# Performance work log

Measured on AMD Instinct MI355X. Metric: run time of the kernel, lower is better.

Reference implementation:

```python
import jax, jax.numpy as jnp
import numpy as np
import math

B, S, N_EMBD, HEAD_SIZE = 32, 2048, 64, 64

def setup_inputs() -> dict:
    key = jax.random.key(0)
    k1, k2, k3, k4 = jax.random.split(key, 4)
    inputs = jax.random.normal(k1, (B, S, N_EMBD), dtype=jnp.float32)
    # nn.Linear(n_embd, head_size, bias=False) weights: shape (head_size, n_embd)
    scale = 1.0 / math.sqrt(N_EMBD)
    Wq = jax.random.normal(k2, (HEAD_SIZE, N_EMBD), dtype=jnp.float32) * scale
    Wk = jax.random.normal(k3, (HEAD_SIZE, N_EMBD), dtype=jnp.float32) * scale
    Wv = jax.random.normal(k4, (HEAD_SIZE, N_EMBD), dtype=jnp.float32) * scale
    return {"inputs": inputs, "Wq": Wq, "Wk": Wk, "Wv": Wv}

def reference(inputs, Wq, Wk, Wv):
    # q, k, v: [B, S, head_size]
    q = jnp.einsum('bse,he->bsh', inputs, Wq)
    k = jnp.einsum('bse,he->bsh', inputs, Wk)
    v = jnp.einsum('bse,he->bsh', inputs, Wv)
    scores = jnp.einsum('bqh,bkh->bqk', q, k) / jnp.sqrt(jnp.float32(HEAD_SIZE))
    # NOTE: the original torch code calls scores.masked_fill(...) out-of-place
    # and discards the result, so NO causal mask is actually applied.
    attention = jax.nn.softmax(scores, axis=-1)
    out = jnp.einsum('bqk,bkh->bqh', attention, v)  # [B, S, head_size]
    return out
```

## Files before the change

kernel.cpp:

```cpp
#include <hip/hip_runtime.h>


#define BATCH 32
#define SEQ   2048
#define HS    64
#define QSCALE 0.18033688011112042f
#define OTS   72
#define MSTR  68

typedef _Float16 f16x8 __attribute__((ext_vector_type(8)));
typedef _Float16 f16x4 __attribute__((ext_vector_type(4)));
typedef float    f32x4 __attribute__((ext_vector_type(4)));
typedef unsigned int u32x4 __attribute__((ext_vector_type(4)));

__global__ __launch_bounds__(256) void prep_w(
    const float* __restrict__ Wq, const float* __restrict__ Wk,
    const float* __restrict__ Wv, _Float16* __restrict__ Wh)
{
    int i = blockIdx.x * 256 + threadIdx.x;
    int rep = i / 12288;
    int j = i - rep * 12288;
    const float* src = (j < 4096) ? Wq : ((j < 8192) ? Wk : Wv);
    float scale = (j < 4096) ? QSCALE : 1.0f;
    Wh[i] = (_Float16)(src[j & 4095] * scale);
}

__global__ __launch_bounds__(256) void proj_kernel(
    const float* __restrict__ x, const _Float16* __restrict__ Wh,
    _Float16* __restrict__ Qh, _Float16* __restrict__ Kh,
    _Float16* __restrict__ Vt)
{
    __shared__ __align__(16) _Float16 ot[64 * OTS];

    const int t    = threadIdx.x;
    const int w    = t >> 6;
    const int lane = t & 63;
    const int lo   = lane & 15;
    const int quad = lane >> 4;
    const long blk0 = (long)blockIdx.x * 64;
    const int  b    = (int)(blk0 / SEQ);
    const int  s0   = (int)(blk0 % SEQ);
    const long rw   = blk0 + w * 16;
    const _Float16* Wrep = Wh + (blockIdx.x & 7) * 12288;

    const float* xp = x + (rw + lo) * HS + quad * 8;
    float4 x0 = *(const float4*)xp;
    float4 x1 = *(const float4*)(xp + 4);
    float4 x2 = *(const float4*)(xp + 32);
    float4 x3 = *(const float4*)(xp + 36);
    f16x8 xb0, xb1;
    xb0[0]=(_Float16)x0.x; xb0[1]=(_Float16)x0.y; xb0[2]=(_Float16)x0.z; xb0[3]=(_Float16)x0.w;
    xb0[4]=(_Float16)x1.x; xb0[5]=(_Float16)x1.y; xb0[6]=(_Float16)x1.z; xb0[7]=(_Float16)x1.w;
    xb1[0]=(_Float16)x2.x; xb1[1]=(_Float16)x2.y; xb1[2]=(_Float16)x2.z; xb1[3]=(_Float16)x2.w;
    xb1[4]=(_Float16)x3.x; xb1[5]=(_Float16)x3.y; xb1[6]=(_Float16)x3.z; xb1[7]=(_Float16)x3.w;

#pragma unroll
    for (int m = 0; m < 3; ++m) {
        const _Float16* Wm = Wrep + m * 4096;
        f32x4 acc[4];
#pragma unroll
        for (int nt = 0; nt < 4; ++nt) { acc[nt][0]=0.f; acc[nt][1]=0.f; acc[nt][2]=0.f; acc[nt][3]=0.f; }
#pragma unroll
        for (int nt = 0; nt < 4; ++nt) {
            f16x8 wa0 = *(const f16x8*)(Wm + (nt * 16 + lo) * 64 + quad * 8);
            f16x8 wa1 = *(const f16x8*)(Wm + (nt * 16 + lo) * 64 + 32 + quad * 8);
            acc[nt] = __builtin_amdgcn_mfma_f32_16x16x32_f16(wa0, xb0, acc[nt], 0, 0, 0);
            acc[nt] = __builtin_amdgcn_mfma_f32_16x16x32_f16(wa1, xb1, acc[nt], 0, 0, 0);
        }
        if (m < 2) {
            _Float16* dst = (m == 0) ? Qh : Kh;
#pragma unroll
            for (int nt = 0; nt < 4; ++nt) {
                f16x4 pk;
                pk[0]=(_Float16)acc[nt][0]; pk[1]=(_Float16)acc[nt][1];
                pk[2]=(_Float16)acc[nt][2]; pk[3]=(_Float16)acc[nt][3];
                *(f16x4*)(dst + (rw + lo) * HS + nt * 16 + quad * 4) = pk;
            }
        } else {
#pragma unroll
            for (int nt = 0; nt < 4; ++nt)
#pragma unroll
                for (int r = 0; r < 4; ++r)
                    ot[(nt * 16 + quad * 4 + r) * OTS + w * 16 + lo] = (_Float16)acc[nt][r];
            __syncthreads();
            const int row = t >> 2, c = t & 3;
            f16x8 r0 = *(const f16x8*)(ot + row * OTS + c * 16);
            f16x8 r1 = *(const f16x8*)(ot + row * OTS + c * 16 + 8);
            _Float16* vd = Vt + ((long)b * HS + row) * SEQ + s0 + c * 16;
            *(f16x8*)vd       = r0;
            *(f16x8*)(vd + 8) = r1;
        }
    }
}

__global__ __launch_bounds__(256, 2) void attn_kernel(
    const _Float16* __restrict__ Q, const _Float16* __restrict__ K,
    const _Float16* __restrict__ Vt, float* __restrict__ out)
{
    __shared__ __align__(16) char smem[65536];
    _Float16* KVb  = (_Float16*)smem;
    float*    obuf = (float*)smem;
    float*    lbuf = obuf + 128 * MSTR;

    const int t    = threadIdx.x;
    const int w    = t >> 6;
    const int lane = t & 63;
    const int lo   = lane & 15;
    const int quad = lane >> 4;
    const int sr   = t >> 2, sc = t & 3;
    const int xr   = lo & 7;

    const int bid = blockIdx.x;
    const int b   = (bid & 7) | ((bid >> 7) << 3);
    const int qt  = (bid >> 3) & 15;
    const int q0  = qt * 128;
    const int qh  = w >> 1;
    const int kh  = w & 1;

    const _Float16* Qb = Q + ((long)b * SEQ + q0 + qh * 64) * HS;
    f16x8 qf[4][2];
#pragma unroll
    for (int q2 = 0; q2 < 4; ++q2) {
        qf[q2][0] = *(const f16x8*)(Qb + (q2 * 16 + lo) * HS + quad * 8);
        qf[q2][1] = *(const f16x8*)(Qb + (q2 * 16 + lo) * HS + 32 + quad * 8);
    }

    const _Float16* Kb = K  + (long)b * SEQ * HS;
    const _Float16* Vb = Vt + (long)b * HS * SEQ;

    const int pr  = (sr & 32) | ((sr & 4) << 2) | ((sr & 24) >> 1) | (sr & 3);
    const int kw0 = pr * 64 + (((2 * sc    ) ^ (pr & 7)) << 3);
    const int kw1 = pr * 64 + (((2 * sc + 1) ^ (pr & 7)) << 3);
    const int vw0 = 4096 + sr * 64 + (((2 * sc    ) ^ (sr & 7)) << 3);
    const int vw1 = 4096 + sr * 64 + (((2 * sc + 1) ^ (sr & 7)) << 3);

    const int kr0 = (kh * 32      + lo) * 64;
    const int kr1 = (kh * 32 + 16 + lo) * 64;
    const int g0  = ((quad    ) ^ xr) << 3;
    const int g1  = ((4 + quad) ^ xr) << 3;
    int voff[4];
#pragma unroll
    for (int ht = 0; ht < 4; ++ht)
        voff[ht] = 4096 + (ht * 16 + lo) * 64 + (((kh * 4 + quad) ^ xr) << 3);

    f32x4 o[4][4], ol[4];
#pragma unroll
    for (int q2 = 0; q2 < 4; ++q2) {
        ol[q2][0]=0.f; ol[q2][1]=0.f; ol[q2][2]=0.f; ol[q2][3]=0.f;
#pragma unroll
        for (int ht = 0; ht < 4; ++ht) { o[q2][ht][0]=0.f; o[q2][ht][1]=0.f; o[q2][ht][2]=0.f; o[q2][ht][3]=0.f; }
    }
    f32x4 zz; zz[0]=0.f; zz[1]=0.f; zz[2]=0.f; zz[3]=0.f;
    f16x8 ones;
#pragma unroll
    for (int j = 0; j < 8; ++j) ones[j] = (_Float16)1.0f;

    const int phase = qt << 1;
    const int key0 = (phase & 31) << 6;
    f16x8 kfA0 = *(const f16x8*)(Kb + (long)(key0 + sr) * HS + sc * 16);
    f16x8 kfB0 = *(const f16x8*)(Kb + (long)(key0 + sr) * HS + sc * 16 + 8);
    f16x8 vfA0 = *(const f16x8*)(Vb + (long)sr * SEQ + key0 + sc * 16);
    f16x8 vfB0 = *(const f16x8*)(Vb + (long)sr * SEQ + key0 + sc * 16 + 8);
    f16x8 kfA1 = *(const f16x8*)(Kb + (long)(key0 + 64 + sr) * HS + sc * 16);
    f16x8 kfB1 = *(const f16x8*)(Kb + (long)(key0 + 64 + sr) * HS + sc * 16 + 8);
    f16x8 vfA1 = *(const f16x8*)(Vb + (long)sr * SEQ + key0 + 64 + sc * 16);
    f16x8 vfB1 = *(const f16x8*)(Vb + (long)sr * SEQ + key0 + 64 + sc * 16 + 8);

    for (int kt2 = 0; kt2 < 16; ++kt2) {
        _Float16* Bp = KVb + (kt2 & 1) * 16384;
        *(f16x8*)(Bp + kw0) = kfA0;
        *(f16x8*)(Bp + kw1) = kfB0;
        *(f16x8*)(Bp + vw0) = vfA0;
        *(f16x8*)(Bp + vw1) = vfB0;
        *(f16x8*)(Bp + 8192 + kw0) = kfA1;
        *(f16x8*)(Bp + 8192 + kw1) = kfB1;
        *(f16x8*)(Bp + 8192 + vw0) = vfA1;
        *(f16x8*)(Bp + 8192 + vw1) = vfB1;

        const int keyn = ((2 * kt2 + 2 + phase) & 31) << 6;
        kfA0 = *(const f16x8*)(Kb + (long)(keyn + sr) * HS + sc * 16);
        kfB0 = *(const f16x8*)(Kb + (long)(keyn + sr) * HS + sc * 16 + 8);
        vfA0 = *(const f16x8*)(Vb + (long)sr * SEQ + keyn + sc * 16);
        vfB0 = *(const f16x8*)(Vb + (long)sr * SEQ + keyn + sc * 16 + 8);
        kfA1 = *(const f16x8*)(Kb + (long)(keyn + 64 + sr) * HS + sc * 16);
        kfB1 = *(const f16x8*)(Kb + (long)(keyn + 64 + sr) * HS + sc * 16 + 8);
        vfA1 = *(const f16x8*)(Vb + (long)sr * SEQ + keyn + 64 + sc * 16);
        vfB1 = *(const f16x8*)(Vb + (long)sr * SEQ + keyn + 64 + sc * 16 + 8);

        __syncthreads();

#pragma unroll
        for (int sub = 0; sub < 2; ++sub) {
            _Float16* Ksp = Bp + sub * 8192;

            f16x8 ka00 = *(const f16x8*)(Ksp + kr0 + g0);
            f16x8 ka01 = *(const f16x8*)(Ksp + kr0 + g1);
            f16x8 ka10 = *(const f16x8*)(Ksp + kr1 + g0);
            f16x8 ka11 = *(const f16x8*)(Ksp + kr1 + g1);

            f16x8 vbf[4];
#pragma unroll
            for (int ht = 0; ht < 4; ++ht)
                vbf[ht] = *(const f16x8*)(Ksp + voff[ht]);

#pragma unroll
            for (int q2 = 0; q2 < 4; ++q2) {
                f32x4 s0, s1;
                s0 = __builtin_amdgcn_mfma_f32_16x16x32_f16(ka00, qf[q2][0], zz, 0, 0, 0);
                s0 = __builtin_amdgcn_mfma_f32_16x16x32_f16(ka01, qf[q2][1], s0, 0, 0, 0);
                s1 = __builtin_amdgcn_mfma_f32_16x16x32_f16(ka10, qf[q2][0], zz, 0, 0, 0);
                s1 = __builtin_amdgcn_mfma_f32_16x16x32_f16(ka11, qf[q2][1], s1, 0, 0, 0);

                u32x4 pw;
                pw[0] = __builtin_bit_cast(unsigned int,
                        __builtin_amdgcn_cvt_pkrtz(__builtin_amdgcn_exp2f(s0[0]),
                                                   __builtin_amdgcn_exp2f(s0[1])));
                pw[1] = __builtin_bit_cast(unsigned int,
                        __builtin_amdgcn_cvt_pkrtz(__builtin_amdgcn_exp2f(s0[2]),
                                                   __builtin_amdgcn_exp2f(s0[3])));
                pw[2] = __builtin_bit_cast(unsigned int,
                        __builtin_amdgcn_cvt_pkrtz(__builtin_amdgcn_exp2f(s1[0]),
                                                   __builtin_amdgcn_exp2f(s1[1])));
                pw[3] = __builtin_bit_cast(unsigned int,
                        __builtin_amdgcn_cvt_pkrtz(__builtin_amdgcn_exp2f(s1[2]),
                                                   __builtin_amdgcn_exp2f(s1[3])));
                f16x8 pa = __builtin_bit_cast(f16x8, pw);

                ol[q2] = __builtin_amdgcn_mfma_f32_16x16x32_f16(pa, ones, ol[q2], 0, 0, 0);
#pragma unroll
                for (int ht = 0; ht < 4; ++ht)
                    o[q2][ht] = __builtin_amdgcn_mfma_f32_16x16x32_f16(pa, vbf[ht], o[q2][ht], 0, 0, 0);
            }
        }
    }

    __syncthreads();
    if (kh == 0) {
#pragma unroll
        for (int q2 = 0; q2 < 4; ++q2) {
#pragma unroll
            for (int ht = 0; ht < 4; ++ht)
#pragma unroll
                for (int r = 0; r < 4; ++r)
                    obuf[(qh * 64 + q2 * 16 + quad * 4 + r) * MSTR + ht * 16 + lo] = o[q2][ht][r];
            if (lo == 0) {
#pragma unroll
                for (int r = 0; r < 4; ++r)
                    lbuf[qh * 64 + q2 * 16 + quad * 4 + r] = ol[q2][r];
            }
        }
    }
    __syncthreads();
    if (kh == 1) {
#pragma unroll
        for (int q2 = 0; q2 < 4; ++q2) {
            float linv[4];
#pragma unroll
            for (int r = 0; r < 4; ++r)
                linv[r] = 1.0f / (lbuf[qh * 64 + q2 * 16 + quad * 4 + r] + ol[q2][r]);
#pragma unroll
            for (int ht = 0; ht < 4; ++ht)
#pragma unroll
                for (int r = 0; r < 4; ++r) {
                    const int row = qh * 64 + q2 * 16 + quad * 4 + r;
                    float v = (obuf[row * MSTR + ht * 16 + lo] + o[q2][ht][r]) * linv[r];
                    out[((long)b * SEQ + q0 + row) * HS + ht * 16 + lo] = v;
                }
        }
    }
}

extern "C" void kernel_launch(void* const* d_in, const int* in_sizes, int n_in,
                              void* d_out, int out_size, void* d_ws, size_t ws_size,
                              hipStream_t stream)
{
    const float* x  = (const float*)d_in[0];
    const float* Wq = (const float*)d_in[1];
    const float* Wk = (const float*)d_in[2];
    const float* Wv = (const float*)d_in[3];
    float* out = (float*)d_out;

    const size_t E = (size_t)BATCH * SEQ * HS;
    _Float16* Qh = (_Float16*)d_ws;
    _Float16* Kh = Qh + E;
    _Float16* Vt = Kh + E;
    _Float16* Wh = Vt + E;

    prep_w<<<384, 256, 0, stream>>>(Wq, Wk, Wv, Wh);
    proj_kernel<<<(BATCH * SEQ) / 64, 256, 0, stream>>>(x, Wh, Qh, Kh, Vt);
    attn_kernel<<<BATCH * (SEQ / 128), 256, 0, stream>>>(Qh, Kh, Vt, out);
}
```

Measured before the change: 127.7 us.

## Split attention key range four ways per 64-query block, single-buffer LDS

Each block now handles 64 queries instead of 128, and its four waves each take a quarter of every 128-key tile, so the work is split along keys instead of queries. Partial outputs and row sums are reduced serially through LDS across the four waves at the end. The K/V staging buffer drops from double to single buffering, which halves shared memory and targets four blocks per CU; the cost is an extra barrier per iteration. The grid doubles to 1024 blocks, so each block's K/V loads now feed half as many queries.

```diff
diff --git a/kernel.cpp b/kernel.cpp
--- a/kernel.cpp
+++ b/kernel.cpp
@@ -93,14 +93,14 @@
     }
 }
 
-__global__ __launch_bounds__(256, 2) void attn_kernel(
+__global__ __launch_bounds__(256, 4) void attn_kernel(
     const _Float16* __restrict__ Q, const _Float16* __restrict__ K,
     const _Float16* __restrict__ Vt, float* __restrict__ out)
 {
-    __shared__ __align__(16) char smem[65536];
+    __shared__ __align__(16) char smem[32768];
     _Float16* KVb  = (_Float16*)smem;
     float*    obuf = (float*)smem;
-    float*    lbuf = obuf + 128 * MSTR;
+    float*    lbuf = obuf + 64 * MSTR;
 
     const int t    = threadIdx.x;
     const int w    = t >> 6;
@@ -111,13 +111,13 @@
     const int xr   = lo & 7;
 
     const int bid = blockIdx.x;
-    const int b   = (bid & 7) | ((bid >> 7) << 3);
-    const int qt  = (bid >> 3) & 15;
-    const int q0  = qt * 128;
-    const int qh  = w >> 1;
+    const int b   = (bid & 7) | ((bid >> 8) << 3);
+    const int qt  = (bid >> 3) & 31;
+    const int q0  = qt * 64;
     const int kh  = w & 1;
-
-    const _Float16* Qb = Q + ((long)b * SEQ + q0 + qh * 64) * HS;
+    const int sub = (w >> 1) & 1;
+
+    const _Float16* Qb = Q + ((long)b * SEQ + q0) * HS;
     f16x8 qf[4][2];
 #pragma unroll
     for (int q2 = 0; q2 < 4; ++q2) {
@@ -155,8 +155,8 @@
 #pragma unroll
     for (int j = 0; j < 8; ++j) ones[j] = (_Float16)1.0f;
 
-    const int phase = qt << 1;
-    const int key0 = (phase & 31) << 6;
+    const int phase = (qt << 1) & 31;
+    const int key0 = phase << 6;
     f16x8 kfA0 = *(const f16x8*)(Kb + (long)(key0 + sr) * HS + sc * 16);
     f16x8 kfB0 = *(const f16x8*)(Kb + (long)(key0 + sr) * HS + sc * 16 + 8);
     f16x8 vfA0 = *(const f16x8*)(Vb + (long)sr * SEQ + key0 + sc * 16);
@@ -167,15 +167,18 @@
     f16x8 vfB1 = *(const f16x8*)(Vb + (long)sr * SEQ + key0 + 64 + sc * 16 + 8);
 
     for (int kt2 = 0; kt2 < 16; ++kt2) {
-        _Float16* Bp = KVb + (kt2 & 1) * 16384;
-        *(f16x8*)(Bp + kw0) = kfA0;
-        *(f16x8*)(Bp + kw1) = kfB0;
-        *(f16x8*)(Bp + vw0) = vfA0;
-        *(f16x8*)(Bp + vw1) = vfB0;
-        *(f16x8*)(Bp + 8192 + kw0) = kfA1;
-        *(f16x8*)(Bp + 8192 + kw1) = kfB1;
-        *(f16x8*)(Bp + 8192 + vw0) = vfA1;
-        *(f16x8*)(Bp + 8192 + vw1) = vfB1;
+        __syncthreads();
+
+        *(f16x8*)(KVb + kw0) = kfA0;
+        *(f16x8*)(KVb + kw1) = kfB0;
+        *(f16x8*)(KVb + vw0) = vfA0;
+        *(f16x8*)(KVb + vw1) = vfB0;
+        *(f16x8*)(KVb + 8192 + kw0) = kfA1;
+        *(f16x8*)(KVb + 8192 + kw1) = kfB1;
+        *(f16x8*)(KVb + 8192 + vw0) = vfA1;
+        *(f16x8*)(KVb + 8192 + vw1) = vfB1;
+
+        __syncthreads();
 
         const int keyn = ((2 * kt2 + 2 + phase) & 31) << 6;
         kfA0 = *(const f16x8*)(Kb + (long)(keyn + sr) * HS + sc * 16);
@@ -187,82 +190,109 @@
         vfA1 = *(const f16x8*)(Vb + (long)sr * SEQ + keyn + 64 + sc * 16);
         vfB1 = *(const f16x8*)(Vb + (long)sr * SEQ + keyn + 64 + sc * 16 + 8);
 
-        __syncthreads();
-
-#pragma unroll
-        for (int sub = 0; sub < 2; ++sub) {
-            _Float16* Ksp = Bp + sub * 8192;
-
-            f16x8 ka00 = *(const f16x8*)(Ksp + kr0 + g0);
-            f16x8 ka01 = *(const f16x8*)(Ksp + kr0 + g1);
-            f16x8 ka10 = *(const f16x8*)(Ksp + kr1 + g0);
-            f16x8 ka11 = *(const f16x8*)(Ksp + kr1 + g1);
-
-            f16x8 vbf[4];
-#pragma unroll
-            for (int ht = 0; ht < 4; ++ht)
-                vbf[ht] = *(const f16x8*)(Ksp + voff[ht]);
-
-#pragma unroll
-            for (int q2 = 0; q2 < 4; ++q2) {
-                f32x4 s0, s1;
-                s0 = __builtin_amdgcn_mfma_f32_16x16x32_f16(ka00, qf[q2][0], zz, 0, 0, 0);
-                s0 = __builtin_amdgcn_mfma_f32_16x16x32_f16(ka01, qf[q2][1], s0, 0, 0, 0);
-                s1 = __builtin_amdgcn_mfma_f32_16x16x32_f16(ka10, qf[q2][0], zz, 0, 0, 0);
-                s1 = __builtin_amdgcn_mfma_f32_16x16x32_f16(ka11, qf[q2][1], s1, 0, 0, 0);
-
-                u32x4 pw;
-                pw[0] = __builtin_bit_cast(unsigned int,
-                        __builtin_amdgcn_cvt_pkrtz(__builtin_amdgcn_exp2f(s0[0]),
-                                                   __builtin_amdgcn_exp2f(s0[1])));
-                pw[1] = __builtin_bit_cast(unsigned int,
-                        __builtin_amdgcn_cvt_pkrtz(__builtin_amdgcn_exp2f(s0[2]),
-                                                   __builtin_amdgcn_exp2f(s0[3])));
-                pw[2] = __builtin_bit_cast(unsigned int,
-                        __builtin_amdgcn_cvt_pkrtz(__builtin_amdgcn_exp2f(s1[0]),
-                                                   __builtin_amdgcn_exp2f(s1[1])));
-                pw[3] = __builtin_bit_cast(unsigned int,
-                        __builtin_amdgcn_cvt_pkrtz(__builtin_amdgcn_exp2f(s1[2]),
-                                                   __builtin_amdgcn_exp2f(s1[3])));
-                f16x8 pa = __builtin_bit_cast(f16x8, pw);
-
-                ol[q2] = __builtin_amdgcn_mfma_f32_16x16x32_f16(pa, ones, ol[q2], 0, 0, 0);
-#pragma unroll
-                for (int ht = 0; ht < 4; ++ht)
-                    o[q2][ht] = __builtin_amdgcn_mfma_f32_16x16x32_f16(pa, vbf[ht], o[q2][ht], 0, 0, 0);
+        _Float16* Ksp = KVb + sub * 8192;
+
+        f16x8 ka00 = *(const f16x8*)(Ksp + kr0 + g0);
+        f16x8 ka01 = *(const f16x8*)(Ksp + kr0 + g1);
+        f16x8 ka10 = *(const f16x8*)(Ksp + kr1 + g0);
+        f16x8 ka11 = *(const f16x8*)(Ksp + kr1 + g1);
+
+        f16x8 vbf[4];
+#pragma unroll
+        for (int ht = 0; ht < 4; ++ht)
+            vbf[ht] = *(const f16x8*)(Ksp + voff[ht]);
+
+#pragma unroll
+        for (int q2 = 0; q2 < 4; ++q2) {
+            f32x4 s0, s1;
+            s0 = __builtin_amdgcn_mfma_f32_16x16x32_f16(ka00, qf[q2][0], zz, 0, 0, 0);
+            s0 = __builtin_amdgcn_mfma_f32_16x16x32_f16(ka01, qf[q2][1], s0, 0, 0, 0);
+            s1 = __builtin_amdgcn_mfma_f32_16x16x32_f16(ka10, qf[q2][0], zz, 0, 0, 0);
+            s1 = __builtin_amdgcn_mfma_f32_16x16x32_f16(ka11, qf[q2][1], s1, 0, 0, 0);
+
+            u32x4 pw;
+            pw[0] = __builtin_bit_cast(unsigned int,
+                    __builtin_amdgcn_cvt_pkrtz(__builtin_amdgcn_exp2f(s0[0]),
+                                               __builtin_amdgcn_exp2f(s0[1])));
+            pw[1] = __builtin_bit_cast(unsigned int,
+                    __builtin_amdgcn_cvt_pkrtz(__builtin_amdgcn_exp2f(s0[2]),
+                                               __builtin_amdgcn_exp2f(s0[3])));
+            pw[2] = __builtin_bit_cast(unsigned int,
+                    __builtin_amdgcn_cvt_pkrtz(__builtin_amdgcn_exp2f(s1[0]),
+                                               __builtin_amdgcn_exp2f(s1[1])));
+            pw[3] = __builtin_bit_cast(unsigned int,
+                    __builtin_amdgcn_cvt_pkrtz(__builtin_amdgcn_exp2f(s1[2]),
+                                               __builtin_amdgcn_exp2f(s1[3])));
+            f16x8 pa = __builtin_bit_cast(f16x8, pw);
+
+            ol[q2] = __builtin_amdgcn_mfma_f32_16x16x32_f16(pa, ones, ol[q2], 0, 0, 0);
+#pragma unroll
+            for (int ht = 0; ht < 4; ++ht)
+                o[q2][ht] = __builtin_amdgcn_mfma_f32_16x16x32_f16(pa, vbf[ht], o[q2][ht], 0, 0, 0);
+        }
+    }
+
+    __syncthreads();
+    if (w == 0) {
+#pragma unroll
+        for (int q2 = 0; q2 < 4; ++q2) {
+#pragma unroll
+            for (int ht = 0; ht < 4; ++ht)
+#pragma unroll
+                for (int r = 0; r < 4; ++r)
+                    obuf[(q2 * 16 + quad * 4 + r) * MSTR + ht * 16 + lo] = o[q2][ht][r];
+            if (lo == 0) {
+#pragma unroll
+                for (int r = 0; r < 4; ++r)
+                    lbuf[q2 * 16 + quad * 4 + r] = ol[q2][r];
             }
         }
     }
-
     __syncthreads();
-    if (kh == 0) {
-#pragma unroll
-        for (int q2 = 0; q2 < 4; ++q2) {
-#pragma unroll
-            for (int ht = 0; ht < 4; ++ht)
-#pragma unroll
-                for (int r = 0; r < 4; ++r)
-                    obuf[(qh * 64 + q2 * 16 + quad * 4 + r) * MSTR + ht * 16 + lo] = o[q2][ht][r];
+    if (w == 1) {
+#pragma unroll
+        for (int q2 = 0; q2 < 4; ++q2) {
+#pragma unroll
+            for (int ht = 0; ht < 4; ++ht)
+#pragma unroll
+                for (int r = 0; r < 4; ++r)
+                    obuf[(q2 * 16 + quad * 4 + r) * MSTR + ht * 16 + lo] += o[q2][ht][r];
             if (lo == 0) {
 #pragma unroll
                 for (int r = 0; r < 4; ++r)
-                    lbuf[qh * 64 + q2 * 16 + quad * 4 + r] = ol[q2][r];
+                    lbuf[q2 * 16 + quad * 4 + r] += ol[q2][r];
             }
         }
     }
     __syncthreads();
-    if (kh == 1) {
+    if (w == 2) {
+#pragma unroll
+        for (int q2 = 0; q2 < 4; ++q2) {
+#pragma unroll
+            for (int ht = 0; ht < 4; ++ht)
+#pragma unroll
+                for (int r = 0; r < 4; ++r)
+                    obuf[(q2 * 16 + quad * 4 + r) * MSTR + ht * 16 + lo] += o[q2][ht][r];
+            if (lo == 0) {
+#pragma unroll
+                for (int r = 0; r < 4; ++r)
+                    lbuf[q2 * 16 + quad * 4 + r] += ol[q2][r];
+            }
+        }
+    }
+    __syncthreads();
+    if (w == 3) {
 #pragma unroll
         for (int q2 = 0; q2 < 4; ++q2) {
             float linv[4];
 #pragma unroll
             for (int r = 0; r < 4; ++r)
-                linv[r] = 1.0f / (lbuf[qh * 64 + q2 * 16 + quad * 4 + r] + ol[q2][r]);
+                linv[r] = 1.0f / (lbuf[q2 * 16 + quad * 4 + r] + ol[q2][r]);
 #pragma unroll
             for (int ht = 0; ht < 4; ++ht)
 #pragma unroll
                 for (int r = 0; r < 4; ++r) {
-                    const int row = qh * 64 + q2 * 16 + quad * 4 + r;
+                    const int row = q2 * 16 + quad * 4 + r;
                     float v = (obuf[row * MSTR + ht * 16 + lo] + o[q2][ht][r]) * linv[r];
                     out[((long)b * SEQ + q0 + row) * HS + ht * 16 + lo] = v;
                 }
@@ -288,5 +318,5 @@
 
     prep_w<<<384, 256, 0, stream>>>(Wq, Wk, Wv, Wh);
     proj_kernel<<<(BATCH * SEQ) / 64, 256, 0, stream>>>(x, Wh, Qh, Kh, Vt);
-    attn_kernel<<<BATCH * (SEQ / 128), 256, 0, stream>>>(Qh, Kh, Vt, out);
+    attn_kernel<<<BATCH * (SEQ / 64), 256, 0, stream>>>(Qh, Kh, Vt, out);
 }
```

New measurement: 327.6 us. 157% more time.
